# Performance work log

Hardware: AMD Instinct MI355X
Metric: run time of the kernel (lower is better)

Reference implementation:

```python
import jax, jax.numpy as jnp
import numpy as np

D = 100      # memory/embedding/time dim
H, C = 2, 50 # heads, per-head channels (out_channels=100 -> 50 per head)
MSG_DIM = 1
EDGE_DIM = D + MSG_DIM  # 101


def setup_inputs() -> dict:
    key = jax.random.key(0)
    ks = jax.random.split(key, 24)
    N, E, B, NUM_NODES = 100000, 500000, 20000, 1000000
    s = 1.0 / np.sqrt(D)
    inp = {
        # node-level memory state and last-update times for the n_id subgraph
        'z': jax.random.normal(ks[0], (N, D), jnp.float32),
        'last_update': jax.random.uniform(ks[1], (N,), jnp.float32) * 1000.0,
        # per-edge event times and raw messages
        't': jax.random.uniform(ks[2], (E,), jnp.float32) * 1000.0,
        'msg': jax.random.normal(ks[3], (E, MSG_DIM), jnp.float32),
        # time encoder: cos(Linear(1 -> D))
        'time_w': jax.random.normal(ks[4], (D, 1), jnp.float32),
        'time_b': jax.random.normal(ks[5], (D,), jnp.float32),
        # TransformerConv linears (in=D, out=H*C=D)
        'Wq': jax.random.normal(ks[6], (D, D), jnp.float32) * s,
        'bq': jnp.zeros((D,), jnp.float32),
        'Wk': jax.random.normal(ks[7], (D, D), jnp.float32) * s,
        'bk': jnp.zeros((D,), jnp.float32),
        'Wv': jax.random.normal(ks[8], (D, D), jnp.float32) * s,
        'bv': jnp.zeros((D,), jnp.float32),
        'We': jax.random.normal(ks[9], (D, EDGE_DIM), jnp.float32) * (1.0 / np.sqrt(EDGE_DIM)),  # lin_edge, no bias
        'Wskip': jax.random.normal(ks[10], (D, D), jnp.float32) * s,
        'bskip': jnp.zeros((D,), jnp.float32),
        # LinkPredictor
        'Wsrc': jax.random.normal(ks[11], (D, D), jnp.float32) * s,
        'bsrc': jnp.zeros((D,), jnp.float32),
        'Wdst': jax.random.normal(ks[12], (D, D), jnp.float32) * s,
        'bdst': jnp.zeros((D,), jnp.float32),
        'Wf': jax.random.normal(ks[13], (1, D), jnp.float32) * s,
        'bf': jnp.zeros((1,), jnp.float32),
        # index structure: n_id are the (unique) global ids of local rows 0..N-1
        'n_id': jnp.arange(N, dtype=jnp.int64) if jax.config.jax_enable_x64 else jnp.arange(N, dtype=jnp.int32),
        'src': jax.random.randint(ks[14], (B,), 0, N),  # global ids present in n_id
        'dst': jax.random.randint(ks[15], (B,), 0, N),
        'edge_index': jax.random.randint(ks[16], (2, E), 0, N),  # local (row) indices
        'num_nodes': NUM_NODES,
    }
    return inp


def reference(z, last_update, t, msg, time_w, time_b,
              Wq, bq, Wk, bk, Wv, bv, We, Wskip, bskip,
              Wsrc, bsrc, Wdst, bdst, Wf, bf,
              n_id, src, dst, edge_index, num_nodes):
    N = z.shape[0]
    # assoc scatter: global id -> local row
    assoc = jnp.zeros((num_nodes,), jnp.int32).at[n_id].set(jnp.arange(N, dtype=jnp.int32))
    src_p = assoc[src]
    dst_p = assoc[dst]

    e_src = edge_index[0]
    e_dst = edge_index[1]

    # --- GraphAttentionEmbedding (TGAT / TransformerConv, eval mode: no dropout) ---
    rel_t = last_update[e_src] - t                                  # [E]
    rel_t_enc = jnp.cos(rel_t[:, None] * time_w[:, 0][None, :] + time_b)  # [E, D]
    edge_attr = jnp.concatenate([rel_t_enc, msg], axis=-1)          # [E, D+1]

    q = (z @ Wq.T + bq).reshape(N, H, C)
    k = (z @ Wk.T + bk).reshape(N, H, C)
    v = (z @ Wv.T + bv).reshape(N, H, C)
    e_proj = (edge_attr @ We.T).reshape(-1, H, C)                   # [E, H, C]

    k_j = k[e_src] + e_proj                                         # [E, H, C]
    alpha = jnp.sum(q[e_dst] * k_j, axis=-1) / jnp.sqrt(jnp.float32(C))  # [E, H]

    # segment softmax over incoming edges of each destination node
    a_max = jax.ops.segment_max(alpha, e_dst, num_segments=N)       # [N, H]
    a = jnp.exp(alpha - a_max[e_dst])
    a_den = jax.ops.segment_sum(a, e_dst, num_segments=N)
    a = a / a_den[e_dst]

    msg_out = (v[e_src] + e_proj) * a[..., None]                    # [E, H, C]
    agg = jax.ops.segment_sum(msg_out, e_dst, num_segments=N).reshape(N, H * C)
    z_out = agg + z @ Wskip.T + bskip                               # root/skip connection

    # --- LinkPredictor ---
    h = jax.nn.relu(z_out[src_p] @ Wsrc.T + bsrc + z_out[dst_p] @ Wdst.T + bdst)
    return h @ Wf.T + bf                                            # [B, 1]
```

## Files before the change

### kernel.cpp

```cpp
#include <hip/hip_runtime.h>
#include <hip/hip_fp16.h>
#include <math.h>

#define TDIM 100
#define EDGED 101
#define EDGEP 104
#define HALFC 50
#define NCOLP 640
#define KPAD 128
#define LDSK 136
#define NCOL2 112
#define K2P 224
#define K2L 232
#define CWS 204
#define SCB 256

typedef __attribute__((ext_vector_type(8))) _Float16 f16x8;
typedef __attribute__((ext_vector_type(4))) float f32x4;

__global__ void k_prep(const int* __restrict__ n_id, int N,
                       int* __restrict__ assoc, int* __restrict__ deg) {
    int i = blockIdx.x * blockDim.x + threadIdx.x;
    if (i < N) {
        assoc[n_id[i]] = i;
        deg[i] = 0;
    }
}

__global__ __launch_bounds__(256) void k_precomp2(
    const float* __restrict__ Wq, const float* __restrict__ bq,
    const float* __restrict__ Wk, const float* __restrict__ bk,
    const float* __restrict__ Wv, const float* __restrict__ bv,
    const float* __restrict__ Ws, const float* __restrict__ bs,
    const float* __restrict__ We,
    __half* __restrict__ WTh, __half* __restrict__ WTl,
    __half* __restrict__ WT2h,
    float* __restrict__ bias_all)
{
    int t = blockIdx.x * blockDim.x + threadIdx.x;
    if (t < NCOLP * KPAD) {
        int col = t >> 7, k = t & 127;
        float val = 0.f;
        if (k < TDIM && col < 602) {
            if (col < 100)      val = Wq[col * TDIM + k];
            else if (col < 200) val = Wk[(col - 100) * TDIM + k];
            else if (col < 300) val = Wv[(col - 200) * TDIM + k];
            else if (col < 400) val = Ws[(col - 300) * TDIM + k];
            else if (col < 501) {
                int j = col - 400;
                for (int d = 0; d < HALFC; ++d)
                    val = fmaf(Wq[d * TDIM + k], We[d * EDGED + j], val);
            } else {
                int j = col - 501;
                for (int d = HALFC; d < TDIM; ++d)
                    val = fmaf(Wq[d * TDIM + k], We[d * EDGED + j], val);
            }
        }
        __half h = __float2half(val);
        WTh[t] = h;
        WTl[t] = __float2half(val - __half2float(h));
        return;
    }
    int t2 = t - NCOLP * KPAD;
    if (t2 < NCOL2 * K2P) {
        int col = t2 / K2P, k = t2 - (t2 / K2P) * K2P;
        float val = 0.f;
        if (col < TDIM) {
            if (k < EDGED && col < HALFC)
                val = We[col * EDGED + k];
            else if (k >= EDGED && k < 2 * EDGED && col >= HALFC)
                val = We[col * EDGED + (k - EDGED)];
        }
        WT2h[t2] = __float2half(val);
        return;
    }
    int i = t2 - NCOL2 * K2P;
    if (i < NCOLP) {
        float b = 0.f;
        if (i < 100)      b = bq[i];
        else if (i < 200) b = bk[i - 100];
        else if (i < 300) b = bv[i - 200];
        else if (i < 400) b = bs[i - 300];
        else if (i < 501) {
            int j = i - 400;
            for (int d = 0; d < HALFC; ++d) b = fmaf(bq[d], We[d * EDGED + j], b);
        } else if (i < 602) {
            int j = i - 501;
            for (int d = HALFC; d < TDIM; ++d) b = fmaf(bq[d], We[d * EDGED + j], b);
        }
        bias_all[i] = b;
    }
}

__global__ void k_count(const int* __restrict__ ei, int E, int* __restrict__ deg) {
    int e = blockIdx.x * blockDim.x + threadIdx.x;
    if (e < E) atomicAdd(&deg[ei[E + e]], 1);
}

__global__ void k_scan1(const int* __restrict__ deg, int N, int* __restrict__ bsum) {
    __shared__ int s[SCB];
    int t = threadIdx.x, i = blockIdx.x * SCB + t;
    s[t] = (i < N) ? deg[i] : 0;
    __syncthreads();
    for (int st = SCB / 2; st > 0; st >>= 1) {
        if (t < st) s[t] += s[t + st];
        __syncthreads();
    }
    if (t == 0) bsum[blockIdx.x] = s[0];
}

__global__ void k_scan2(const int* __restrict__ bsum, int nb, int* __restrict__ bbase) {
    __shared__ int s[512];
    int t = threadIdx.x;
    int v = (t < nb) ? bsum[t] : 0;
    s[t] = v;
    __syncthreads();
    for (int st = 1; st < 512; st <<= 1) {
        int x = (t >= st) ? s[t - st] : 0;
        __syncthreads();
        s[t] += x;
        __syncthreads();
    }
    if (t < nb) bbase[t] = s[t] - v;
}

__global__ void k_scan3(const int* __restrict__ deg, int N,
                        const int* __restrict__ bbase,
                        int* __restrict__ off, int* __restrict__ cursor) {
    __shared__ int s[SCB];
    int t = threadIdx.x, i = blockIdx.x * SCB + t;
    int v = (i < N) ? deg[i] : 0;
    s[t] = v;
    __syncthreads();
    for (int st = 1; st < SCB; st <<= 1) {
        int x = (t >= st) ? s[t - st] : 0;
        __syncthreads();
        s[t] += x;
        __syncthreads();
    }
    if (i < N) {
        int o = bbase[blockIdx.x] + s[t] - v;
        off[i] = o;
        cursor[i] = o;
    }
}

__global__ void k_fill2(const int* __restrict__ ei,
                        const float* __restrict__ lu, const float* __restrict__ tt,
                        const float* __restrict__ msg, int E,
                        int* __restrict__ cursor,
                        int* __restrict__ esrcs, int* __restrict__ edst,
                        float2* __restrict__ aux_rm) {
    int e = blockIdx.x * blockDim.x + threadIdx.x;
    if (e >= E) return;
    int sn = ei[e], dn = ei[E + e];
    int pos = atomicAdd(&cursor[dn], 1);
    esrcs[pos] = sn;
    edst[pos] = dn;
    aux_rm[pos] = make_float2(lu[sn] - tt[e], msg[e]);
}

__global__ __launch_bounds__(256) void k_gemm(
    const float* __restrict__ z,
    const __half* __restrict__ WTh,
    const float* __restrict__ bias_all,
    __half* __restrict__ qh, __half* __restrict__ kh, __half* __restrict__ vh,
    float* __restrict__ zbuf, __half* __restrict__ qW0h, __half* __restrict__ qW1h,
    int N)
{
    __shared__ __half zsh[64][LDSK];
    __shared__ __half zsl[64][LDSK];
    int tid = threadIdx.x;
    int m0 = blockIdx.x * 64;
    int cols0 = blockIdx.y * 80;

    for (int idx = tid; idx < 64 * 25; idx += 256) {
        int row = idx / 25, c4 = idx % 25;
        int node = m0 + row;
        float4 zz = (node < N) ? ((const float4*)(z + (size_t)node * TDIM))[c4]
                               : make_float4(0.f, 0.f, 0.f, 0.f);
        __half2 h01 = __floats2half2_rn(zz.x, zz.y);
        __half2 h23 = __floats2half2_rn(zz.z, zz.w);
        float2 f01 = __half22float2(h01);
        float2 f23 = __half22float2(h23);
        *(__half2*)&zsh[row][c4 * 4]     = h01;
        *(__half2*)&zsh[row][c4 * 4 + 2] = h23;
        *(__half2*)&zsl[row][c4 * 4]     = __floats2half2_rn(zz.x - f01.x, zz.y - f01.y);
        *(__half2*)&zsl[row][c4 * 4 + 2] = __floats2half2_rn(zz.z - f23.x, zz.w - f23.y);
    }
    for (int idx = tid; idx < 64 * 28; idx += 256) {
        int row = idx / 28, k = TDIM + idx % 28;
        zsh[row][k] = __half(0.f);
        zsl[row][k] = __half(0.f);
    }
    __syncthreads();

    int wave = tid >> 6, lane = tid & 63;
    int arow = wave * 16 + (lane & 15);
    int kgrp = (lane >> 4) * 8;
    f32x4 acc[5];
#pragma unroll
    for (int c = 0; c < 5; ++c) acc[c] = f32x4{0.f, 0.f, 0.f, 0.f};

#pragma unroll
    for (int kk = 0; kk < KPAD; kk += 32) {
        f16x8 ah = *(const f16x8*)&zsh[arow][kk + kgrp];
        f16x8 al = *(const f16x8*)&zsl[arow][kk + kgrp];
#pragma unroll
        for (int c = 0; c < 5; ++c) {
            int col = cols0 + c * 16 + (lane & 15);
            f16x8 bh = *(const f16x8*)&WTh[col * KPAD + kk + kgrp];
            acc[c] = __builtin_amdgcn_mfma_f32_16x16x32_f16(ah, bh, acc[c], 0, 0, 0);
            acc[c] = __builtin_amdgcn_mfma_f32_16x16x32_f16(al, bh, acc[c], 0, 0, 0);
        }
    }

#pragma unroll
    for (int c = 0; c < 5; ++c) {
        int col = cols0 + c * 16 + (lane & 15);
        if (col >= 602) continue;
        float bias = bias_all[col];
#pragma unroll
        for (int r = 0; r < 4; ++r) {
            int node = m0 + wave * 16 + (lane >> 4) * 4 + r;
            if (node >= N) continue;
            float val = acc[c][r] + bias;
            if (col < 100)      qh[(size_t)node * TDIM + col]          = __float2half(val);
            else if (col < 200) kh[(size_t)node * TDIM + col - 100]    = __float2half(val);
            else if (col < 300) vh[(size_t)node * TDIM + col - 200]    = __float2half(val);
            else if (col < 400) zbuf[(size_t)node * TDIM + col - 300]  = val;
            else if (col < 501) qW0h[(size_t)node * EDGEP + col - 400] = __float2half(val);
            else                qW1h[(size_t)node * EDGEP + col - 501] = __float2half(val);
        }
    }
}

__global__ __launch_bounds__(256) void k_logit2(
    const float2* __restrict__ aux_rm,
    const int* __restrict__ esrcs, const int* __restrict__ edst,
    const float* __restrict__ tw, const float* __restrict__ tb,
    const __half* __restrict__ qh, const __half* __restrict__ kh,
    const __half* __restrict__ qW0h, const __half* __restrict__ qW1h,
    int E, float4* __restrict__ aux_s)
{
    const float INVS = 0.14142135623730951f;
    int p = blockIdx.x * 256 + threadIdx.x;
    if (p >= E) return;
    float2 rm = aux_rm[p];
    int sn = esrcs[p], dn = edst[p];
    float rel = rm.x, m = rm.y;

    const __half2* q2 = (const __half2*)(qh + (size_t)dn * TDIM);
    const __half2* k2 = (const __half2*)(kh + (size_t)sn * TDIM);
    float qk0 = 0.f, qk1 = 0.f;
#pragma unroll
    for (int c = 0; c < 25; ++c) {
        float2 qq = __half22float2(q2[c]);
        float2 kk = __half22float2(k2[c]);
        qk0 = fmaf(qq.x, kk.x, qk0);
        qk0 = fmaf(qq.y, kk.y, qk0);
    }
#pragma unroll
    for (int c = 25; c < 50; ++c) {
        float2 qq = __half22float2(q2[c]);
        float2 kk = __half22float2(k2[c]);
        qk1 = fmaf(qq.x, kk.x, qk1);
        qk1 = fmaf(qq.y, kk.y, qk1);
    }

    const __half2* w02 = (const __half2*)(qW0h + (size_t)dn * EDGEP);
    const __half2* w12 = (const __half2*)(qW1h + (size_t)dn * EDGEP);
    float l0 = qk0, l1 = qk1;
#pragma unroll 5
    for (int c = 0; c < 50; ++c) {
        float cv0 = __cosf(fmaf(rel, tw[2 * c], tb[2 * c]));
        float cv1 = __cosf(fmaf(rel, tw[2 * c + 1], tb[2 * c + 1]));
        float2 w0 = __half22float2(w02[c]);
        float2 w1 = __half22float2(w12[c]);
        l0 = fmaf(w0.x, cv0, l0); l0 = fmaf(w0.y, cv1, l0);
        l1 = fmaf(w1.x, cv0, l1); l1 = fmaf(w1.y, cv1, l1);
    }
    l0 = fmaf(__half2float(qW0h[(size_t)dn * EDGEP + 100]), m, l0);
    l1 = fmaf(__half2float(qW1h[(size_t)dn * EDGEP + 100]), m, l1);

    aux_s[p] = make_float4(rel, m, __expf(l0 * INVS), __expf(l1 * INVS));
}

__global__ __launch_bounds__(256) void k_gather3(
    const float* __restrict__ tw, const float* __restrict__ tb,
    const __half* __restrict__ vh, const int* __restrict__ esrcs,
    const float4* __restrict__ aux_s,
    const int* __restrict__ off, const int* __restrict__ deg,
    int N, float* __restrict__ zbuf, float* __restrict__ CW)
{
    int gw = (blockIdx.x * 256 + threadIdx.x) >> 6;
    int lane = threadIdx.x & 63;
    int n = gw / 6;
    int role = gw - n * 6;
    if (n >= N) return;
    int dg = deg[n], nb = off[n];

    if (role < 2) {
        int d = role * 64 + lane;
        bool act = d < TDIM;
        bool h1 = d >= HALFC;
        float acc = 0.f, den = 0.f;
        for (int i = 0; i < dg; ++i) {
            float4 ax = aux_s[nb + i];
            int sn = esrcs[nb + i];
            float a = h1 ? ax.w : ax.z;
            den += a;
            if (act) acc = fmaf(a, __half2float(vh[(size_t)sn * TDIM + d]), acc);
        }
        if (dg > 0 && act) zbuf[(size_t)n * TDIM + d] += acc / den;
    } else {
        int r2 = role - 2;
        int hh = r2 >> 1, sub = r2 & 1;
        int j = sub * 64 + lane;
        bool act = j < EDGED;
        float twj = (j < TDIM) ? tw[j] : 0.f;
        float tbj = (j < TDIM) ? tb[j] : 0.f;
        float acc = 0.f, den = 0.f;
        for (int i = 0; i < dg; ++i) {
            float4 ax = aux_s[nb + i];
            float a = hh ? ax.w : ax.z;
            den += a;
            float cv = (j < TDIM) ? __cosf(fmaf(ax.x, twj, tbj)) : ax.y;
            acc = fmaf(a, cv, acc);
        }
        if (act) CW[(size_t)n * CWS + hh * EDGED + j] = (dg > 0) ? acc / den : 0.f;
    }
}

__global__ __launch_bounds__(256) void k_gemmCW(
    const float* __restrict__ CW,
    const __half* __restrict__ WT2h,
    int N, float* __restrict__ zbuf)
{
    __shared__ __half ash[64][K2L];
    __shared__ __half asl[64][K2L];
    int tid = threadIdx.x;
    int m0 = blockIdx.x * 64;

    for (int idx = tid; idx < 64 * K2P; idx += 256) {
        int row = idx / K2P, k = idx - (idx / K2P) * K2P;
        int node = m0 + row;
        float vv = (k < 2 * EDGED && node < N) ? CW[(size_t)node * CWS + k] : 0.f;
        __half h = __float2half(vv);
        ash[row][k] = h;
        asl[row][k] = __float2half(vv - __half2float(h));
    }
    __syncthreads();

    int wave = tid >> 6, lane = tid & 63;
    int arow = wave * 16 + (lane & 15);
    int kgrp = (lane >> 4) * 8;
    f32x4 acc[7];
#pragma unroll
    for (int c = 0; c < 7; ++c) acc[c] = f32x4{0.f, 0.f, 0.f, 0.f};

#pragma unroll
    for (int kk = 0; kk < K2P; kk += 32) {
        f16x8 ah = *(const f16x8*)&ash[arow][kk + kgrp];
        f16x8 al = *(const f16x8*)&asl[arow][kk + kgrp];
#pragma unroll
        for (int c = 0; c < 7; ++c) {
            int col = c * 16 + (lane & 15);
            f16x8 bh = *(const f16x8*)&WT2h[col * K2P + kk + kgrp];
            acc[c] = __builtin_amdgcn_mfma_f32_16x16x32_f16(ah, bh, acc[c], 0, 0, 0);
            acc[c] = __builtin_amdgcn_mfma_f32_16x16x32_f16(al, bh, acc[c], 0, 0, 0);
        }
    }

#pragma unroll
    for (int c = 0; c < 7; ++c) {
        int col = c * 16 + (lane & 15);
        if (col >= TDIM) continue;
#pragma unroll
        for (int r = 0; r < 4; ++r) {
            int node = m0 + wave * 16 + (lane >> 4) * 4 + r;
            if (node >= N) continue;
            size_t o = (size_t)node * TDIM + col;
            zbuf[o] += acc[c][r];
        }
    }
}

#define LPB 64
__global__ __launch_bounds__(256) void k_link(
    const float* __restrict__ zout,
    const float* __restrict__ Wsr, const float* __restrict__ bsr,
    const float* __restrict__ Wds, const float* __restrict__ bds,
    const float* __restrict__ Wf, const float* __restrict__ bf,
    const int* __restrict__ assoc, const int* __restrict__ src,
    const int* __restrict__ dst, int B, float* __restrict__ outp)
{
    __shared__ float zs[LPB][EDGED];
    __shared__ float zd[LPB][EDGED];
    __shared__ int rowS[LPB], rowD[LPB];
    int tid = threadIdx.x;
    int l0 = blockIdx.x * LPB;
    if (tid < LPB) {
        int li = l0 + tid;
        rowS[tid] = (li < B) ? assoc[src[li]] : 0;
        rowD[tid] = (li < B) ? assoc[dst[li]] : 0;
    }
    __syncthreads();
    for (int i = tid; i < LPB * TDIM; i += 256) {
        int l = i / TDIM, d2 = i - l * TDIM;
        zs[l][d2] = zout[(size_t)rowS[l] * TDIM + d2];
        zd[l][d2] = zout[(size_t)rowD[l] * TDIM + d2];
    }
    __syncthreads();
    int l = tid >> 2, qt = tid & 3;
    float part = 0.f;
    for (int oo = 0; oo < 25; ++oo) {
        int out = qt * 25 + oo;
        const float4* ws4 = (const float4*)(Wsr + out * TDIM);
        const float4* wd4 = (const float4*)(Wds + out * TDIM);
        float accS = 0.f, accD = 0.f;
#pragma unroll
        for (int j = 0; j < 25; ++j) {
            float4 a = ws4[j];
            float4 b = wd4[j];
            accS = fmaf(a.x, zs[l][4*j+0], accS); accS = fmaf(a.y, zs[l][4*j+1], accS);
            accS = fmaf(a.z, zs[l][4*j+2], accS); accS = fmaf(a.w, zs[l][4*j+3], accS);
            accD = fmaf(b.x, zd[l][4*j+0], accD); accD = fmaf(b.y, zd[l][4*j+1], accD);
            accD = fmaf(b.z, zd[l][4*j+2], accD); accD = fmaf(b.w, zd[l][4*j+3], accD);
        }
        float h = accS + accD + bsr[out] + bds[out];
        h = fmaxf(h, 0.f);
        part = fmaf(Wf[out], h, part);
    }
    part += __shfl_xor(part, 1);
    part += __shfl_xor(part, 2);
    int li = l0 + l;
    if (qt == 0 && li < B) outp[li] = part + bf[0];
}

extern "C" void kernel_launch(void* const* d_in, const int* in_sizes, int n_in,
                              void* d_out, int out_size, void* d_ws, size_t ws_size,
                              hipStream_t stream)
{
    const float* z   = (const float*)d_in[0];
    const float* lu  = (const float*)d_in[1];
    const float* tt  = (const float*)d_in[2];
    const float* msg = (const float*)d_in[3];
    const float* tw  = (const float*)d_in[4];
    const float* tb  = (const float*)d_in[5];
    const float* Wq  = (const float*)d_in[6];  const float* bq  = (const float*)d_in[7];
    const float* Wk  = (const float*)d_in[8];  const float* bk  = (const float*)d_in[9];
    const float* Wv  = (const float*)d_in[10]; const float* bv  = (const float*)d_in[11];
    const float* We  = (const float*)d_in[12];
    const float* Wsk = (const float*)d_in[13]; const float* bsk = (const float*)d_in[14];
    const float* Wsr = (const float*)d_in[15]; const float* bsr = (const float*)d_in[16];
    const float* Wds = (const float*)d_in[17]; const float* bds = (const float*)d_in[18];
    const float* Wf  = (const float*)d_in[19]; const float* bf  = (const float*)d_in[20];
    const int* n_id  = (const int*)d_in[21];
    const int* srcI  = (const int*)d_in[22];
    const int* dstI  = (const int*)d_in[23];
    const int* ei    = (const int*)d_in[24];

    int N = in_sizes[0] / TDIM;
    int E = in_sizes[2];
    int B = in_sizes[22];
    const size_t NUM_NODES = 1000000;
    int nblk = (N + SCB - 1) / SCB;

    char* w = (char*)d_ws;
    int*    assoc = (int*)w;    w += NUM_NODES * sizeof(int);
    float2* auxrm = (float2*)w; w += (size_t)E * 8;
    float4* aux_s = (float4*)w; w += (size_t)E * 16;
    int*    esrcs = (int*)w;    w += (size_t)E * 4;
    int*    edst  = (int*)w;    w += (size_t)E * 4;
    __half* vh    = (__half*)w; w += (size_t)N * TDIM * 2;
    float*  zbuf  = (float*)w;  w += (size_t)N * TDIM * 4;
    char*   uni   = w;
    __half* qh    = (__half*)uni;
    __half* kh    = (__half*)(uni + (size_t)N * TDIM * 2);
    __half* qW0h  = (__half*)(uni + (size_t)N * TDIM * 4);
    __half* qW1h  = (__half*)(uni + (size_t)N * TDIM * 4 + (size_t)N * EDGEP * 2);
    float*  CW    = (float*)uni;
    w += (size_t)N * CWS * 4;
    __half* WTh   = (__half*)w; w += (size_t)NCOLP * KPAD * 2;
    __half* WTl   = (__half*)w; w += (size_t)NCOLP * KPAD * 2;
    __half* WT2h  = (__half*)w; w += (size_t)NCOL2 * K2P * 2;
    float*  biasA = (float*)w;  w += NCOLP * 4;
    int*    deg   = (int*)w;    w += (size_t)N * sizeof(int);
    int*    off   = (int*)w;    w += (size_t)N * sizeof(int);
    int*    curs  = (int*)w;    w += (size_t)N * sizeof(int);
    int*    bsum  = (int*)w;    w += 512 * sizeof(int);
    int*    bbase = (int*)w;    w += 512 * sizeof(int);

    hipLaunchKernelGGL(k_prep, dim3((N + 255) / 256), dim3(256), 0, stream,
                       n_id, N, assoc, deg);
    hipLaunchKernelGGL(k_precomp2,
                       dim3((NCOLP * KPAD + NCOL2 * K2P + NCOLP + 255) / 256), dim3(256), 0, stream,
                       Wq, bq, Wk, bk, Wv, bv, Wsk, bsk, We, WTh, WTl, WT2h, biasA);
    hipLaunchKernelGGL(k_count, dim3((E + 255) / 256), dim3(256), 0, stream, ei, E, deg);
    hipLaunchKernelGGL(k_scan1, dim3(nblk), dim3(SCB), 0, stream, deg, N, bsum);
    hipLaunchKernelGGL(k_scan2, dim3(1), dim3(512), 0, stream, bsum, nblk, bbase);
    hipLaunchKernelGGL(k_scan3, dim3(nblk), dim3(SCB), 0, stream, deg, N, bbase, off, curs);
    hipLaunchKernelGGL(k_fill2, dim3((E + 255) / 256), dim3(256), 0, stream,
                       ei, lu, tt, msg, E, curs, esrcs, edst, auxrm);
    hipLaunchKernelGGL(k_gemm, dim3((N + 63) / 64, 8), dim3(256), 0, stream,
                       z, WTh, biasA, qh, kh, vh, zbuf, qW0h, qW1h, N);
    hipLaunchKernelGGL(k_logit2, dim3((E + 255) / 256), dim3(256), 0, stream,
                       auxrm, esrcs, edst, tw, tb, qh, kh, qW0h, qW1h, E, aux_s);
    hipLaunchKernelGGL(k_gather3, dim3(((size_t)N * 6 + 3) / 4), dim3(256), 0, stream,
                       tw, tb, vh, esrcs, aux_s, off, deg, N, zbuf, CW);
    hipLaunchKernelGGL(k_gemmCW, dim3((N + 63) / 64), dim3(256), 0, stream,
                       CW, WT2h, N, zbuf);
    hipLaunchKernelGGL(k_link, dim3((B + LPB - 1) / LPB), dim3(256), 0, stream,
                       zbuf, Wsr, bsr, Wds, bds, Wf, bf, assoc, srcI, dstI, B,
                       (float*)d_out);
}
```

Baseline: 1.118 ms.

## Store softmax-weighted edge features as fp16 and drop split-precision GEMM pass

The gather kernel now uses one 256-thread block per node, with four waves: two for value aggregation and two for edge-feature aggregation. Each edge-feature wave computes both heads at once, so each cosine is evaluated once and reused for both heads. The edge loops are unrolled by four to keep more loads in flight. The weighted edge features are written as fp16 instead of fp32, and the follow-up MFMA GEMM drops the low-part correction pass, halving its MFMA count and LDS use. The cost is lower accuracy in the edge-projection contribution.

```diff
diff --git a/kernel.cpp b/kernel.cpp
--- a/kernel.cpp
+++ b/kernel.cpp
@@ -12,7 +12,7 @@
 #define NCOL2 112
 #define K2P 224
 #define K2L 232
-#define CWS 204
+#define CWS2 208
 #define SCB 256
 
 typedef __attribute__((ext_vector_type(8))) _Float16 f16x8;
@@ -286,18 +286,16 @@
     aux_s[p] = make_float4(rel, m, __expf(l0 * INVS), __expf(l1 * INVS));
 }
 
-__global__ __launch_bounds__(256) void k_gather3(
+__global__ __launch_bounds__(256) void k_gather4(
     const float* __restrict__ tw, const float* __restrict__ tb,
     const __half* __restrict__ vh, const int* __restrict__ esrcs,
     const float4* __restrict__ aux_s,
     const int* __restrict__ off, const int* __restrict__ deg,
-    int N, float* __restrict__ zbuf, float* __restrict__ CW)
-{
-    int gw = (blockIdx.x * 256 + threadIdx.x) >> 6;
+    int N, float* __restrict__ zbuf, __half* __restrict__ CWh)
+{
+    int n = blockIdx.x;
+    int role = threadIdx.x >> 6;
     int lane = threadIdx.x & 63;
-    int n = gw / 6;
-    int role = gw - n * 6;
-    if (n >= N) return;
     int dg = deg[n], nb = off[n];
 
     if (role < 2) {
@@ -305,50 +303,84 @@
         bool act = d < TDIM;
         bool h1 = d >= HALFC;
         float acc = 0.f, den = 0.f;
-        for (int i = 0; i < dg; ++i) {
-            float4 ax = aux_s[nb + i];
-            int sn = esrcs[nb + i];
+        const float4* ap = aux_s + nb;
+        const int* sp = esrcs + nb;
+        int i = 0;
+        for (; i + 4 <= dg; i += 4) {
+            float4 ax0 = ap[i], ax1 = ap[i + 1], ax2 = ap[i + 2], ax3 = ap[i + 3];
+            int s0 = sp[i], s1 = sp[i + 1], s2 = sp[i + 2], s3 = sp[i + 3];
+            float v0 = act ? __half2float(vh[(size_t)s0 * TDIM + d]) : 0.f;
+            float v1 = act ? __half2float(vh[(size_t)s1 * TDIM + d]) : 0.f;
+            float v2 = act ? __half2float(vh[(size_t)s2 * TDIM + d]) : 0.f;
+            float v3 = act ? __half2float(vh[(size_t)s3 * TDIM + d]) : 0.f;
+            float a0 = h1 ? ax0.w : ax0.z;
+            float a1 = h1 ? ax1.w : ax1.z;
+            float a2 = h1 ? ax2.w : ax2.z;
+            float a3 = h1 ? ax3.w : ax3.z;
+            den += (a0 + a1) + (a2 + a3);
+            acc = fmaf(a0, v0, acc); acc = fmaf(a1, v1, acc);
+            acc = fmaf(a2, v2, acc); acc = fmaf(a3, v3, acc);
+        }
+        for (; i < dg; ++i) {
+            float4 ax = ap[i];
+            int s = sp[i];
             float a = h1 ? ax.w : ax.z;
             den += a;
-            if (act) acc = fmaf(a, __half2float(vh[(size_t)sn * TDIM + d]), acc);
+            if (act) acc = fmaf(a, __half2float(vh[(size_t)s * TDIM + d]), acc);
         }
         if (dg > 0 && act) zbuf[(size_t)n * TDIM + d] += acc / den;
     } else {
-        int r2 = role - 2;
-        int hh = r2 >> 1, sub = r2 & 1;
-        int j = sub * 64 + lane;
+        int j = (role - 2) * 64 + lane;
         bool act = j < EDGED;
+        bool isMsg = (j == TDIM);
         float twj = (j < TDIM) ? tw[j] : 0.f;
         float tbj = (j < TDIM) ? tb[j] : 0.f;
-        float acc = 0.f, den = 0.f;
-        for (int i = 0; i < dg; ++i) {
-            float4 ax = aux_s[nb + i];
-            float a = hh ? ax.w : ax.z;
-            den += a;
-            float cv = (j < TDIM) ? __cosf(fmaf(ax.x, twj, tbj)) : ax.y;
-            acc = fmaf(a, cv, acc);
-        }
-        if (act) CW[(size_t)n * CWS + hh * EDGED + j] = (dg > 0) ? acc / den : 0.f;
+        float acc0 = 0.f, acc1 = 0.f, den0 = 0.f, den1 = 0.f;
+        const float4* ap = aux_s + nb;
+        int i = 0;
+        for (; i + 4 <= dg; i += 4) {
+            float4 ax0 = ap[i], ax1 = ap[i + 1], ax2 = ap[i + 2], ax3 = ap[i + 3];
+            float cv0 = isMsg ? ax0.y : __cosf(fmaf(ax0.x, twj, tbj));
+            float cv1 = isMsg ? ax1.y : __cosf(fmaf(ax1.x, twj, tbj));
+            float cv2 = isMsg ? ax2.y : __cosf(fmaf(ax2.x, twj, tbj));
+            float cv3 = isMsg ? ax3.y : __cosf(fmaf(ax3.x, twj, tbj));
+            den0 += (ax0.z + ax1.z) + (ax2.z + ax3.z);
+            den1 += (ax0.w + ax1.w) + (ax2.w + ax3.w);
+            acc0 = fmaf(ax0.z, cv0, acc0); acc0 = fmaf(ax1.z, cv1, acc0);
+            acc0 = fmaf(ax2.z, cv2, acc0); acc0 = fmaf(ax3.z, cv3, acc0);
+            acc1 = fmaf(ax0.w, cv0, acc1); acc1 = fmaf(ax1.w, cv1, acc1);
+            acc1 = fmaf(ax2.w, cv2, acc1); acc1 = fmaf(ax3.w, cv3, acc1);
+        }
+        for (; i < dg; ++i) {
+            float4 ax = ap[i];
+            float cv = isMsg ? ax.y : __cosf(fmaf(ax.x, twj, tbj));
+            den0 += ax.z; den1 += ax.w;
+            acc0 = fmaf(ax.z, cv, acc0);
+            acc1 = fmaf(ax.w, cv, acc1);
+        }
+        if (act) {
+            __half r0 = __float2half((dg > 0) ? acc0 / den0 : 0.f);
+            __half r1 = __float2half((dg > 0) ? acc1 / den1 : 0.f);
+            CWh[(size_t)n * CWS2 + j] = r0;
+            CWh[(size_t)n * CWS2 + EDGED + j] = r1;
+        }
     }
 }
 
 __global__ __launch_bounds__(256) void k_gemmCW(
-    const float* __restrict__ CW,
+    const __half* __restrict__ CWh,
     const __half* __restrict__ WT2h,
     int N, float* __restrict__ zbuf)
 {
     __shared__ __half ash[64][K2L];
-    __shared__ __half asl[64][K2L];
     int tid = threadIdx.x;
     int m0 = blockIdx.x * 64;
 
     for (int idx = tid; idx < 64 * K2P; idx += 256) {
         int row = idx / K2P, k = idx - (idx / K2P) * K2P;
         int node = m0 + row;
-        float vv = (k < 2 * EDGED && node < N) ? CW[(size_t)node * CWS + k] : 0.f;
-        __half h = __float2half(vv);
-        ash[row][k] = h;
-        asl[row][k] = __float2half(vv - __half2float(h));
+        ash[row][k] = (k < 2 * EDGED && node < N) ? CWh[(size_t)node * CWS2 + k]
+                                                  : __half(0.f);
     }
     __syncthreads();
 
@@ -362,13 +394,11 @@
 #pragma unroll
     for (int kk = 0; kk < K2P; kk += 32) {
         f16x8 ah = *(const f16x8*)&ash[arow][kk + kgrp];
-        f16x8 al = *(const f16x8*)&asl[arow][kk + kgrp];
 #pragma unroll
         for (int c = 0; c < 7; ++c) {
             int col = c * 16 + (lane & 15);
             f16x8 bh = *(const f16x8*)&WT2h[col * K2P + kk + kgrp];
             acc[c] = __builtin_amdgcn_mfma_f32_16x16x32_f16(ah, bh, acc[c], 0, 0, 0);
-            acc[c] = __builtin_amdgcn_mfma_f32_16x16x32_f16(al, bh, acc[c], 0, 0, 0);
         }
     }
 
@@ -480,8 +510,8 @@
     __half* kh    = (__half*)(uni + (size_t)N * TDIM * 2);
     __half* qW0h  = (__half*)(uni + (size_t)N * TDIM * 4);
     __half* qW1h  = (__half*)(uni + (size_t)N * TDIM * 4 + (size_t)N * EDGEP * 2);
-    float*  CW    = (float*)uni;
-    w += (size_t)N * CWS * 4;
+    __half* CWh   = (__half*)uni;
+    w += (size_t)N * TDIM * 4 + (size_t)N * EDGEP * 4;
     __half* WTh   = (__half*)w; w += (size_t)NCOLP * KPAD * 2;
     __half* WTl   = (__half*)w; w += (size_t)NCOLP * KPAD * 2;
     __half* WT2h  = (__half*)w; w += (size_t)NCOL2 * K2P * 2;
@@ -507,10 +537,10 @@
                        z, WTh, biasA, qh, kh, vh, zbuf, qW0h, qW1h, N);
     hipLaunchKernelGGL(k_logit2, dim3((E + 255) / 256), dim3(256), 0, stream,
                        auxrm, esrcs, edst, tw, tb, qh, kh, qW0h, qW1h, E, aux_s);
-    hipLaunchKernelGGL(k_gather3, dim3(((size_t)N * 6 + 3) / 4), dim3(256), 0, stream,
-                       tw, tb, vh, esrcs, aux_s, off, deg, N, zbuf, CW);
+    hipLaunchKernelGGL(k_gather4, dim3(N), dim3(256), 0, stream,
+                       tw, tb, vh, esrcs, aux_s, off, deg, N, zbuf, CWh);
     hipLaunchKernelGGL(k_gemmCW, dim3((N + 63) / 64), dim3(256), 0, stream,
-                       CW, WT2h, N, zbuf);
+                       CWh, WT2h, N, zbuf);
     hipLaunchKernelGGL(k_link, dim3((B + LPB - 1) / LPB), dim3(256), 0, stream,
                        zbuf, Wsr, bsr, Wds, bds, Wf, bf, assoc, srcI, dstI, B,
                        (float*)d_out);
```

Measured after the change: 898.6 us. 19.6% less time.
